# Performance work log

Measured on AMD Instinct MI355X. Metric: run time of the kernel, lower is better.

## Reference

```python
import jax, jax.numpy as jnp
import numpy as np

HIDDEN = 2048
NUM_HEADS = 16
HEAD_DIM = 128
WINDOW = 256
BATCH = 2
SEQ = 2048
ROPE_BASE = 10000.0


def apply_rope(t):
    # t: [b, h, s, d]; half-split (rotate-half) rotary embedding
    d = t.shape[-1]
    s = t.shape[-2]
    inv_freq = 1.0 / (ROPE_BASE ** (jnp.arange(0, d, 2, dtype=jnp.float32) / d))  # [d/2]
    freqs = jnp.arange(s, dtype=jnp.float32)[:, None] * inv_freq[None, :]          # [s, d/2]
    cos, sin = jnp.cos(freqs), jnp.sin(freqs)
    t1, t2 = t[..., : d // 2], t[..., d // 2 :]
    return jnp.concatenate([t1 * cos - t2 * sin, t1 * sin + t2 * cos], axis=-1)


def setup_inputs() -> dict:
    key = jax.random.key(0)
    ks = jax.random.split(key, 10)
    dm = HEAD_DIM * NUM_HEADS
    lin_std = 1.0 / np.sqrt(HIDDEN)
    out_std = 1.0 / np.sqrt(dm)
    return {
        "x": jax.random.normal(ks[0], (BATCH, SEQ, HIDDEN), dtype=jnp.float32),
        "W_Q": jax.random.uniform(ks[1], (HIDDEN, dm), jnp.float32, -lin_std, lin_std),
        "b_Q": jax.random.uniform(ks[2], (dm,), jnp.float32, -lin_std, lin_std),
        "W_K": jax.random.uniform(ks[3], (HIDDEN, dm), jnp.float32, -lin_std, lin_std),
        "b_K": jax.random.uniform(ks[4], (dm,), jnp.float32, -lin_std, lin_std),
        "W_V": jax.random.uniform(ks[5], (HIDDEN, dm), jnp.float32, -lin_std, lin_std),
        "b_V": jax.random.uniform(ks[6], (dm,), jnp.float32, -lin_std, lin_std),
        "W_O": jax.random.uniform(ks[7], (dm, HIDDEN), jnp.float32, -out_std, out_std),
        "b_O": jax.random.uniform(ks[8], (HIDDEN,), jnp.float32, -out_std, out_std),
        "key_weights": jax.random.normal(ks[9], (NUM_HEADS,), dtype=jnp.float32),
    }


def reference(x, W_Q, b_Q, W_K, b_K, W_V, b_V, W_O, b_O, key_weights):
    b, s, _ = x.shape
    scale = HEAD_DIM ** -0.5

    def split_heads(t):  # [b, s, h*d] -> [b, h, s, d]
        return t.reshape(b, s, NUM_HEADS, HEAD_DIM).transpose(0, 2, 1, 3)

    q = split_heads(x @ W_Q + b_Q)
    k = split_heads(x @ W_K + b_K)
    v = split_heads(x @ W_V + b_V)

    q = apply_rope(q)
    k = apply_rope(k)

    # num_kv_heads == num_heads here, so group_size == 1: plain per-head attention
    scores = jnp.einsum("bhqd,bhkd->bhqk", q, k) * scale
    scores = scores * key_weights[None, :, None, None]

    # sliding-window causal mask: allow 0 <= i - j <= WINDOW
    i = jnp.arange(s)[:, None]
    j = jnp.arange(s)[None, :]
    allowed = (j <= i) & (j >= i - WINDOW)
    scores = jnp.where(allowed[None, None], scores, -jnp.inf)

    attn = jax.nn.softmax(scores, axis=-1)
    out = jnp.einsum("bhqk,bhkd->bhqd", attn, v)  # [b, h, s, d]
    out = out.transpose(0, 2, 1, 3).reshape(b, s, NUM_HEADS * HEAD_DIM)
    return out @ W_O + b_O
```

## Files before the change

kernel.cpp:

```cpp
#include <hip/hip_runtime.h>
#include <cstdint>

#define SEQn   2048
#define NHn    16
#define HDn    128
#define DMn    2048
#define HIDn   2048
#define BATCHn 2
#define WINn   256
#define MROWS  (BATCHn*SEQn)
#define WELEMS ((size_t)HIDn * DMn)

typedef short s16x8 __attribute__((ext_vector_type(8)));
typedef float f32x4 __attribute__((ext_vector_type(4)));

__device__ __forceinline__ float bf2f(ushort x) {
    union { uint u; float f; } v; v.u = ((uint)x) << 16; return v.f;
}
__device__ __forceinline__ ushort f2bf(float f) {
    union { float f; uint u; } v; v.f = f;
    uint u = v.u;
    return (ushort)((u + 0x7FFFu + ((u >> 16) & 1u)) >> 16);
}

#define GLOAD_LDS16(g, l) __builtin_amdgcn_global_load_lds(                   \
    (const __attribute__((address_space(1))) unsigned int*)(g),               \
    (__attribute__((address_space(3))) unsigned int*)(l), 16, 0, 0)

#define FENCE() do { asm volatile("" ::: "memory");                           \
                     __builtin_amdgcn_sched_barrier(0); } while (0)

__global__ __launch_bounds__(256)
void transpose_all_kernel(const float* __restrict__ WQ, const float* __restrict__ WK,
                          const float* __restrict__ WV, const float* __restrict__ WO,
                          ushort* __restrict__ WT,
                          const float* __restrict__ x, ushort* __restrict__ xb)
{
    const int tid = threadIdx.y * 32 + threadIdx.x;
    if (blockIdx.z == 4) {
        const int bid = blockIdx.y * 64 + blockIdx.x;
        const size_t base = ((size_t)bid * 256 + tid) * 8;
        const float4 a0 = *reinterpret_cast<const float4*>(x + base);
        const float4 a1 = *reinterpret_cast<const float4*>(x + base + 4);
        ushort4 o0, o1;
        o0.x = f2bf(a0.x); o0.y = f2bf(a0.y); o0.z = f2bf(a0.z); o0.w = f2bf(a0.w);
        o1.x = f2bf(a1.x); o1.y = f2bf(a1.y); o1.z = f2bf(a1.z); o1.w = f2bf(a1.w);
        *reinterpret_cast<ushort4*>(xb + base)     = o0;
        *reinterpret_cast<ushort4*>(xb + base + 4) = o1;
        return;
    }
    __shared__ ushort t[32][33];
    const float* src = (blockIdx.z == 0) ? WQ : (blockIdx.z == 1) ? WK
                     : (blockIdx.z == 2) ? WV : WO;
    ushort* dst = WT + (size_t)blockIdx.z * WELEMS;
    const int tx = threadIdx.x, ty = threadIdx.y;
    const int n  = blockIdx.x * 32 + tx;
    const int k0 = blockIdx.y * 32;
    #pragma unroll
    for (int r = ty; r < 32; r += 8)
        t[r][tx] = f2bf(src[(size_t)(k0 + r) * 2048 + n]);
    __syncthreads();
    const int k  = k0 + tx;
    const int nb = blockIdx.x * 32;
    #pragma unroll
    for (int r = ty; r < 32; r += 8)
        dst[(size_t)(nb + r) * 2048 + k] = t[tx][r];
}

__global__ __launch_bounds__(256)
void transpose_cvt_kernel(const float* __restrict__ src, ushort* __restrict__ dst)
{
    __shared__ ushort t[32][33];
    const int tx = threadIdx.x, ty = threadIdx.y;
    const int n  = blockIdx.x * 32 + tx;
    const int k0 = blockIdx.y * 32;
    #pragma unroll
    for (int r = ty; r < 32; r += 8)
        t[r][tx] = f2bf(src[(size_t)(k0 + r) * 2048 + n]);
    __syncthreads();
    const int k  = k0 + tx;
    const int nb = blockIdx.x * 32;
    #pragma unroll
    for (int r = ty; r < 32; r += 8)
        dst[(size_t)(nb + r) * 2048 + k] = t[tx][r];
}

template<int ABF16>
__global__ __launch_bounds__(256)
void gemm_qkv_kernel(const void* __restrict__ Araw, const ushort* __restrict__ WT,
                     const float* __restrict__ bQ, const float* __restrict__ bK,
                     const float* __restrict__ bV,
                     ushort* __restrict__ Qb, ushort* __restrict__ Kb,
                     ushort* __restrict__ Vt)
{
    __shared__ __align__(16) ushort smem[32768];
    const int tid = threadIdx.x;
    const int m0  = blockIdx.y * 128;
    const int n0g = blockIdx.x * 128;
    const int sel = n0g >> 11;
    const int n0  = n0g & 2047;
    const ushort* BT  = WT + (size_t)sel * WELEMS;
    const float* bias = (sel == 0) ? bQ : (sel == 1) ? bK : bV;
    const int w  = tid >> 6;
    const int l  = tid & 63;
    const int wy = w >> 1, wx = w & 1;
    const int q  = l >> 4, lm = l & 15;
    const int sw = lm & 7;

    f32x4 acc[4][4];
    #pragma unroll
    for (int i = 0; i < 4; ++i)
        #pragma unroll
        for (int j = 0; j < 4; ++j) acc[i][j] = (f32x4)0.0f;

    auto stage = [&](int slot, int kt) {
        ushort* AsS = smem + slot * 16384;
        ushort* BsS = AsS + 8192;
        if (ABF16) {
            #pragma unroll
            for (int it = 0; it < 4; ++it) {
                const int v = it * 256 + tid;
                const int r = v >> 3;
                const int cs = ((v & 7) ^ (r & 7)) << 3;
                const ushort* gA = (const ushort*)Araw + (size_t)(m0 + r) * HIDn + kt + cs;
                const ushort* gB = BT + (size_t)(n0 + r) * HIDn + kt + cs;
                GLOAD_LDS16(gA, AsS + (it * 256 + w * 64) * 8);
                GLOAD_LDS16(gB, BsS + (it * 256 + w * 64) * 8);
            }
        } else {
            #pragma unroll
            for (int it = 0; it < 4; ++it) {
                const int v = it * 256 + tid;
                const int r = v >> 3;
                const int c = (v & 7) << 3;
                const float* Af = (const float*)Araw + (size_t)(m0 + r) * HIDn + kt + c;
                const float4 a0 = *reinterpret_cast<const float4*>(Af);
                const float4 a1 = *reinterpret_cast<const float4*>(Af + 4);
                ushort* d = &AsS[(size_t)(v ^ (r & 7)) * 8];
                d[0] = f2bf(a0.x); d[1] = f2bf(a0.y); d[2] = f2bf(a0.z); d[3] = f2bf(a0.w);
                d[4] = f2bf(a1.x); d[5] = f2bf(a1.y); d[6] = f2bf(a1.z); d[7] = f2bf(a1.w);
                const int cs = ((v & 7) ^ (r & 7)) << 3;
                const ushort* gB = BT + (size_t)(n0 + r) * HIDn + kt + cs;
                GLOAD_LDS16(gB, BsS + (it * 256 + w * 64) * 8);
            }
        }
    };

    auto compute = [&](int slot) {
        const ushort* AsS = smem + slot * 16384;
        const ushort* BsS = AsS + 8192;
        #pragma unroll
        for (int ks = 0; ks < 2; ++ks) {
            s16x8 af[4], bfv[4];
            #pragma unroll
            for (int im = 0; im < 4; ++im) {
                const int arow = wy * 64 + im * 16 + lm;
                af[im] = *reinterpret_cast<const s16x8*>(
                    &AsS[arow * 64 + (((ks * 4 + q) ^ sw) << 3)]);
            }
            #pragma unroll
            for (int in = 0; in < 4; ++in) {
                const int brow = wx * 64 + in * 16 + lm;
                bfv[in] = *reinterpret_cast<const s16x8*>(
                    &BsS[brow * 64 + (((ks * 4 + q) ^ sw) << 3)]);
            }
            __builtin_amdgcn_s_setprio(1);
            #pragma unroll
            for (int im = 0; im < 4; ++im)
                #pragma unroll
                for (int in = 0; in < 4; ++in)
                    acc[im][in] = __builtin_amdgcn_mfma_f32_16x16x32_bf16(af[im], bfv[in], acc[im][in], 0, 0, 0);
            __builtin_amdgcn_s_setprio(0);
        }
    };

    const int NT = HIDn / 64;
    stage(0, 0);
    int cur = 0;
    for (int t = 0; t < NT - 1; ++t) {
        stage(cur ^ 1, (t + 1) * 64);
        if (ABF16) asm volatile("s_waitcnt vmcnt(8)" ::: "memory");
        else       asm volatile("s_waitcnt vmcnt(4)" ::: "memory");
        __builtin_amdgcn_s_barrier();
        FENCE();
        compute(cur);
        FENCE();
        if (!ABF16) asm volatile("s_waitcnt lgkmcnt(0)" ::: "memory");
        __builtin_amdgcn_s_barrier();
        FENCE();
        cur ^= 1;
    }
    asm volatile("s_waitcnt vmcnt(0)" ::: "memory");
    __builtin_amdgcn_s_barrier();
    FENCE();
    compute(cur);
    __syncthreads();

    if (sel == 2) {
        ushort* ctile = smem;
        #pragma unroll
        for (int in = 0; in < 4; ++in) {
            const int col = wx * 64 + in * 16 + lm;
            const float bv = bias[n0 + col];
            #pragma unroll
            for (int im = 0; im < 4; ++im) {
                const int row0 = wy * 64 + im * 16 + q * 4;
                #pragma unroll
                for (int r = 0; r < 4; ++r)
                    ctile[col * 136 + row0 + r] = f2bf(acc[im][in][r] + bv);
            }
        }
        __syncthreads();
        const int hh = n0 >> 7;
        const int bb = m0 >> 11;
        const int s0 = m0 & (SEQn - 1);
        const int st = (tid & 15) * 8;
        const int d0 = tid >> 4;
        #pragma unroll
        for (int db = 0; db < 8; ++db) {
            const int d = d0 + db * 16;
            const ushort4 v0 = *reinterpret_cast<const ushort4*>(&ctile[d * 136 + st]);
            const ushort4 v1 = *reinterpret_cast<const ushort4*>(&ctile[d * 136 + st + 4]);
            ushort* dstp = Vt + (((size_t)(bb * NHn + hh)) * HDn + d) * SEQn + s0 + st;
            *reinterpret_cast<ushort4*>(dstp)     = v0;
            *reinterpret_cast<ushort4*>(dstp + 4) = v1;
        }
    } else {
        ushort* ctile = smem;
        #pragma unroll
        for (int in = 0; in < 4; ++in) {
            const int col = wx * 64 + in * 16 + lm;
            const float bv = bias[n0 + col];
            #pragma unroll
            for (int im = 0; im < 4; ++im) {
                const int row0 = wy * 64 + im * 16 + q * 4;
                #pragma unroll
                for (int r = 0; r < 4; ++r)
                    ctile[(row0 + r) * 136 + col] = f2bf(acc[im][in][r] + bv);
            }
        }
        __syncthreads();
        ushort* dst = (sel == 0) ? Qb : Kb;
        const int d = tid & 63;
        const float invf = exp2f(-(float)d * 0.20762050593046f);
        for (int r = tid >> 6; r < 128; r += 4) {
            const int s = (m0 + r) & (SEQn - 1);
            const float ang = (float)s * invf;
            float sn, cs;
            __sincosf(ang, &sn, &cs);
            const float t1 = bf2f(ctile[r * 136 + d]);
            const float t2 = bf2f(ctile[r * 136 + 64 + d]);
            const size_t base = (size_t)(m0 + r) * DMn + n0 + d;
            dst[base]      = f2bf(t1 * cs - t2 * sn);
            dst[base + 64] = f2bf(t1 * sn + t2 * cs);
        }
    }
}

__global__ __launch_bounds__(256)
void gemm_out_kernel(const ushort* __restrict__ A, const ushort* __restrict__ BT,
                     const float* __restrict__ bias, float* __restrict__ C)
{
    __shared__ __align__(16) ushort smem[24576];
    const int tid = threadIdx.x;
    const int m0 = blockIdx.y * 64;
    const int n0 = blockIdx.x * 128;
    const int w  = tid >> 6;
    const int l  = tid & 63;
    const int wy = w >> 1, wx = w & 1;
    const int q  = l >> 4, lm = l & 15;
    const int sw = lm & 7;

    f32x4 acc[2][4];
    #pragma unroll
    for (int i = 0; i < 2; ++i)
        #pragma unroll
        for (int j = 0; j < 4; ++j) acc[i][j] = (f32x4)0.0f;

    auto stage = [&](int slot, int kt) {
        ushort* AsS = smem + slot * 12288;
        ushort* BsS = AsS + 4096;
        #pragma unroll
        for (int it = 0; it < 2; ++it) {
            const int v = it * 256 + tid;
            const int r = v >> 3;
            const int cs = ((v & 7) ^ (r & 7)) << 3;
            GLOAD_LDS16(A + (size_t)(m0 + r) * DMn + kt + cs,
                        AsS + (it * 256 + w * 64) * 8);
        }
        #pragma unroll
        for (int it = 0; it < 4; ++it) {
            const int v = it * 256 + tid;
            const int r = v >> 3;
            const int cs = ((v & 7) ^ (r & 7)) << 3;
            GLOAD_LDS16(BT + (size_t)(n0 + r) * DMn + kt + cs,
                        BsS + (it * 256 + w * 64) * 8);
        }
    };

    auto compute = [&](int slot) {
        const ushort* AsS = smem + slot * 12288;
        const ushort* BsS = AsS + 4096;
        #pragma unroll
        for (int ks = 0; ks < 2; ++ks) {
            s16x8 af[2], bfv[4];
            #pragma unroll
            for (int im = 0; im < 2; ++im) {
                const int arow = wy * 32 + im * 16 + lm;
                af[im] = *reinterpret_cast<const s16x8*>(
                    &AsS[arow * 64 + (((ks * 4 + q) ^ sw) << 3)]);
            }
            #pragma unroll
            for (int in = 0; in < 4; ++in) {
                const int brow = wx * 64 + in * 16 + lm;
                bfv[in] = *reinterpret_cast<const s16x8*>(
                    &BsS[brow * 64 + (((ks * 4 + q) ^ sw) << 3)]);
            }
            __builtin_amdgcn_s_setprio(1);
            #pragma unroll
            for (int im = 0; im < 2; ++im)
                #pragma unroll
                for (int in = 0; in < 4; ++in)
                    acc[im][in] = __builtin_amdgcn_mfma_f32_16x16x32_bf16(af[im], bfv[in], acc[im][in], 0, 0, 0);
            __builtin_amdgcn_s_setprio(0);
        }
    };

    const int NT = DMn / 64;
    stage(0, 0);
    int cur = 0;
    for (int t = 0; t < NT - 1; ++t) {
        stage(cur ^ 1, (t + 1) * 64);
        asm volatile("s_waitcnt vmcnt(6)" ::: "memory");
        __builtin_amdgcn_s_barrier();
        FENCE();
        compute(cur);
        FENCE();
        __builtin_amdgcn_s_barrier();
        FENCE();
        cur ^= 1;
    }
    asm volatile("s_waitcnt vmcnt(0)" ::: "memory");
    __builtin_amdgcn_s_barrier();
    FENCE();
    compute(cur);

    #pragma unroll
    for (int in = 0; in < 4; ++in) {
        const int gcol = n0 + wx * 64 + in * 16 + lm;
        const float bv = bias[gcol];
        #pragma unroll
        for (int im = 0; im < 2; ++im) {
            const int grow0 = m0 + wy * 32 + im * 16 + q * 4;
            #pragma unroll
            for (int r = 0; r < 4; ++r)
                C[(size_t)(grow0 + r) * HIDn + gcol] = acc[im][in][r] + bv;
        }
    }
}

__global__ __launch_bounds__(256)
void attn_mfma_kernel(const ushort* Q, const ushort* __restrict__ K,
                      const ushort* __restrict__ Vt, const float* __restrict__ kw,
                      ushort* AO)
{
    __shared__ ushort plds[4][16 * 40];
    const int w  = threadIdx.x >> 6;
    const int l  = threadIdx.x & 63;
    const int q  = l >> 4, lm = l & 15;
    const int gw = blockIdx.x * 4 + w;
    const int qt = gw & 127;
    const int h  = (gw >> 7) & (NHn - 1);
    const int b  = gw >> 11;
    const int q0 = qt * 16;
    const float f = kw[h] * 0.08838834764831845f;

    s16x8 qf[4];
    const size_t qbase = ((size_t)(b * SEQn + q0 + lm)) * DMn + h * HDn;
    #pragma unroll
    for (int ks = 0; ks < 4; ++ks)
        qf[ks] = *reinterpret_cast<const s16x8*>(Q + qbase + ks * 32 + q * 8);

    f32x4 O[8];
    #pragma unroll
    for (int nt = 0; nt < 8; ++nt) O[nt] = (f32x4)0.0f;
    float m[4]    = {-1e30f, -1e30f, -1e30f, -1e30f};
    float lsum[4] = {0.f, 0.f, 0.f, 0.f};

    const int lo = q0 - WINn;
    const int c0 = lo > 0 ? (lo & ~31) : 0;
    const int nch = (q0 + 16 - c0 + 31) >> 5;

    const size_t kbh = ((size_t)(b * SEQn)) * DMn + h * HDn;
    const size_t vbh = ((size_t)(b * NHn + h)) * HDn * SEQn;

    for (int c = 0; c < nch; ++c) {
        const int kc = c0 + c * 32;
        s16x8 vf[8];
        #pragma unroll
        for (int nt = 0; nt < 8; ++nt)
            vf[nt] = *reinterpret_cast<const s16x8*>(
                Vt + vbh + (size_t)(nt * 16 + lm) * SEQn + kc + q * 8);
        f32x4 S[2];
        #pragma unroll
        for (int t = 0; t < 2; ++t) {
            f32x4 acc = (f32x4)0.0f;
            const size_t krow = kbh + (size_t)(kc + t * 16 + lm) * DMn;
            s16x8 kf[4];
            #pragma unroll
            for (int ks = 0; ks < 4; ++ks)
                kf[ks] = *reinterpret_cast<const s16x8*>(K + krow + ks * 32 + q * 8);
            __builtin_amdgcn_s_setprio(1);
            #pragma unroll
            for (int ks = 0; ks < 4; ++ks)
                acc = __builtin_amdgcn_mfma_f32_16x16x32_bf16(qf[ks], kf[ks], acc, 0, 0, 0);
            __builtin_amdgcn_s_setprio(0);
            S[t] = acc;
        }
        const int j0 = kc + lm, j1 = kc + 16 + lm;
        #pragma unroll
        for (int r = 0; r < 4; ++r) {
            const int i = q0 + q * 4 + r;
            float v0 = S[0][r] * f;
            float v1 = S[1][r] * f;
            if (j0 > i || j0 < i - WINn) v0 = -1e30f;
            if (j1 > i || j1 < i - WINn) v1 = -1e30f;
            float mx = fmaxf(v0, v1);
            #pragma unroll
            for (int off = 8; off > 0; off >>= 1)
                mx = fmaxf(mx, __shfl_xor(mx, off));
            const float mn = fmaxf(m[r], mx);
            const float alpha = __expf(m[r] - mn);
            m[r] = mn;
            const ushort h0 = f2bf(__expf(v0 - mn));
            const ushort h1 = f2bf(__expf(v1 - mn));
            plds[w][(q * 4 + r) * 40 + lm]      = h0;
            plds[w][(q * 4 + r) * 40 + 16 + lm] = h1;
            float ps = bf2f(h0) + bf2f(h1);
            #pragma unroll
            for (int off = 8; off > 0; off >>= 1)
                ps += __shfl_xor(ps, off);
            lsum[r] = lsum[r] * alpha + ps;
            #pragma unroll
            for (int nt = 0; nt < 8; ++nt) O[nt][r] *= alpha;
        }
        const s16x8 pf = *reinterpret_cast<const s16x8*>(&plds[w][lm * 40 + q * 8]);
        __builtin_amdgcn_s_setprio(1);
        #pragma unroll
        for (int nt = 0; nt < 8; ++nt)
            O[nt] = __builtin_amdgcn_mfma_f32_16x16x32_bf16(pf, vf[nt], O[nt], 0, 0, 0);
        __builtin_amdgcn_s_setprio(0);
    }
    #pragma unroll
    for (int r = 0; r < 4; ++r) {
        const float inv = 1.0f / lsum[r];
        const size_t orow = ((size_t)(b * SEQn + q0 + q * 4 + r)) * DMn + h * HDn;
        #pragma unroll
        for (int nt = 0; nt < 8; ++nt)
            AO[orow + nt * 16 + lm] = f2bf(O[nt][r] * inv);
    }
}

extern "C" void kernel_launch(void* const* d_in, const int* in_sizes, int n_in,
                              void* d_out, int out_size, void* d_ws, size_t ws_size,
                              hipStream_t stream)
{
    (void)in_sizes; (void)n_in; (void)out_size;
    const float* x  = (const float*)d_in[0];
    const float* WQ = (const float*)d_in[1];
    const float* bQ = (const float*)d_in[2];
    const float* WK = (const float*)d_in[3];
    const float* bK = (const float*)d_in[4];
    const float* WV = (const float*)d_in[5];
    const float* bV = (const float*)d_in[6];
    const float* WO = (const float*)d_in[7];
    const float* bO = (const float*)d_in[8];
    const float* kw = (const float*)d_in[9];
    float* out = (float*)d_out;

    char* ws = (char*)d_ws;
    const size_t AELEMS = (size_t)MROWS * DMn;
    ushort* Qb = (ushort*)ws;
    ushort* Kb = (ushort*)(ws + AELEMS * 2);
    ushort* Vt = (ushort*)(ws + AELEMS * 4);
    ushort* WT = (ushort*)(ws + AELEMS * 6);
    const size_t FULL = AELEMS * 6 + WELEMS * 8 + AELEMS * 2;
    const bool have_full = ws_size >= FULL;
    ushort* xb = (ushort*)(ws + AELEMS * 6 + WELEMS * 8);

    const dim3 tblk(32, 8);

    if (have_full) {
        transpose_all_kernel<<<dim3(64, 64, 5), tblk, 0, stream>>>(WQ, WK, WV, WO, WT, x, xb);
        gemm_qkv_kernel<1><<<dim3(3 * DMn / 128, MROWS / 128), 256, 0, stream>>>(
            xb, WT, bQ, bK, bV, Qb, Kb, Vt);
        attn_mfma_kernel<<<dim3(BATCHn * NHn * (SEQn / 16) / 4), 256, 0, stream>>>(Qb, Kb, Vt, kw, Qb);
        gemm_out_kernel<<<dim3(HIDn / 128, MROWS / 64), 256, 0, stream>>>(
            Qb, WT + 3 * WELEMS, bO, out);
    } else {
        transpose_all_kernel<<<dim3(64, 64, 3), tblk, 0, stream>>>(WQ, WK, WV, WO, WT, x, xb);
        gemm_qkv_kernel<0><<<dim3(3 * DMn / 128, MROWS / 128), 256, 0, stream>>>(
            x, WT, bQ, bK, bV, Qb, Kb, Vt);
        attn_mfma_kernel<<<dim3(BATCHn * NHn * (SEQn / 16) / 4), 256, 0, stream>>>(Qb, Kb, Vt, kw, Qb);
        transpose_cvt_kernel<<<dim3(64, 64), tblk, 0, stream>>>(WO, WT);
        gemm_out_kernel<<<dim3(HIDn / 128, MROWS / 64), 256, 0, stream>>>(Qb, WT, bO, out);
    }
}
```

Measured before the change: 374.5 us.

## Widen transpose tiles, enlarge out-GEMM tile, add block swizzles across kernels

```diff
diff --git a/kernel.cpp b/kernel.cpp
--- a/kernel.cpp
+++ b/kernel.cpp
@@ -38,33 +38,43 @@
 {
     const int tid = threadIdx.y * 32 + threadIdx.x;
     if (blockIdx.z == 4) {
-        const int bid = blockIdx.y * 64 + blockIdx.x;
-        const size_t base = ((size_t)bid * 256 + tid) * 8;
-        const float4 a0 = *reinterpret_cast<const float4*>(x + base);
-        const float4 a1 = *reinterpret_cast<const float4*>(x + base + 4);
-        ushort4 o0, o1;
-        o0.x = f2bf(a0.x); o0.y = f2bf(a0.y); o0.z = f2bf(a0.z); o0.w = f2bf(a0.w);
-        o1.x = f2bf(a1.x); o1.y = f2bf(a1.y); o1.z = f2bf(a1.z); o1.w = f2bf(a1.w);
-        *reinterpret_cast<ushort4*>(xb + base)     = o0;
-        *reinterpret_cast<ushort4*>(xb + base + 4) = o1;
+        const int bid = blockIdx.y * 32 + blockIdx.x;
+        const size_t b0 = (size_t)bid * 8192;
+        #pragma unroll
+        for (int i = 0; i < 4; ++i) {
+            const size_t base = b0 + i * 2048 + tid * 8;
+            const float4 a0 = *reinterpret_cast<const float4*>(x + base);
+            const float4 a1 = *reinterpret_cast<const float4*>(x + base + 4);
+            ushort4 o0, o1;
+            o0.x = f2bf(a0.x); o0.y = f2bf(a0.y); o0.z = f2bf(a0.z); o0.w = f2bf(a0.w);
+            o1.x = f2bf(a1.x); o1.y = f2bf(a1.y); o1.z = f2bf(a1.z); o1.w = f2bf(a1.w);
+            *reinterpret_cast<ushort4*>(xb + base)     = o0;
+            *reinterpret_cast<ushort4*>(xb + base + 4) = o1;
+        }
         return;
     }
-    __shared__ ushort t[32][33];
+    __shared__ ushort t[64][72];
     const float* src = (blockIdx.z == 0) ? WQ : (blockIdx.z == 1) ? WK
                      : (blockIdx.z == 2) ? WV : WO;
     ushort* dst = WT + (size_t)blockIdx.z * WELEMS;
-    const int tx = threadIdx.x, ty = threadIdx.y;
-    const int n  = blockIdx.x * 32 + tx;
-    const int k0 = blockIdx.y * 32;
-    #pragma unroll
-    for (int r = ty; r < 32; r += 8)
-        t[r][tx] = f2bf(src[(size_t)(k0 + r) * 2048 + n]);
+    const int n0 = blockIdx.x * 64;
+    const int k0 = blockIdx.y * 64;
+    const int c  = tid & 63;
+    const int rr = tid >> 6;
+    #pragma unroll
+    for (int i = 0; i < 16; ++i) {
+        const int r = i * 4 + rr;
+        t[c][r] = f2bf(src[(size_t)(k0 + r) * 2048 + n0 + c]);
+    }
     __syncthreads();
-    const int k  = k0 + tx;
-    const int nb = blockIdx.x * 32;
-    #pragma unroll
-    for (int r = ty; r < 32; r += 8)
-        dst[(size_t)(nb + r) * 2048 + k] = t[tx][r];
+    const int rowg = tid >> 4;
+    const int kc   = (tid & 15) * 4;
+    #pragma unroll
+    for (int rr2 = 0; rr2 < 4; ++rr2) {
+        const int arow = rowg + rr2 * 16;
+        const ushort4 v = *reinterpret_cast<const ushort4*>(&t[arow][kc]);
+        *reinterpret_cast<ushort4*>(dst + (size_t)(n0 + arow) * 2048 + k0 + kc) = v;
+    }
 }
 
 __global__ __launch_bounds__(256)
@@ -95,8 +105,10 @@
 {
     __shared__ __align__(16) ushort smem[32768];
     const int tid = threadIdx.x;
-    const int m0  = blockIdx.y * 128;
-    const int n0g = blockIdx.x * 128;
+    const int lin = blockIdx.y * 48 + blockIdx.x;
+    const int swz = (lin & 7) * 192 + (lin >> 3);
+    const int m0  = (swz / 48) * 128;
+    const int n0g = (swz % 48) * 128;
     const int sel = n0g >> 11;
     const int n0  = n0g & 2047;
     const ushort* BT  = WT + (size_t)sel * WELEMS;
@@ -261,52 +273,48 @@
 void gemm_out_kernel(const ushort* __restrict__ A, const ushort* __restrict__ BT,
                      const float* __restrict__ bias, float* __restrict__ C)
 {
-    __shared__ __align__(16) ushort smem[24576];
+    __shared__ __align__(16) ushort smem[32768];
     const int tid = threadIdx.x;
-    const int m0 = blockIdx.y * 64;
-    const int n0 = blockIdx.x * 128;
+    const int lin = blockIdx.y * 16 + blockIdx.x;
+    const int swz = (lin & 7) * 64 + (lin >> 3);
+    const int m0 = (swz >> 4) * 128;
+    const int n0 = (swz & 15) * 128;
     const int w  = tid >> 6;
     const int l  = tid & 63;
     const int wy = w >> 1, wx = w & 1;
     const int q  = l >> 4, lm = l & 15;
     const int sw = lm & 7;
 
-    f32x4 acc[2][4];
-    #pragma unroll
-    for (int i = 0; i < 2; ++i)
+    f32x4 acc[4][4];
+    #pragma unroll
+    for (int i = 0; i < 4; ++i)
         #pragma unroll
         for (int j = 0; j < 4; ++j) acc[i][j] = (f32x4)0.0f;
 
     auto stage = [&](int slot, int kt) {
-        ushort* AsS = smem + slot * 12288;
-        ushort* BsS = AsS + 4096;
-        #pragma unroll
-        for (int it = 0; it < 2; ++it) {
-            const int v = it * 256 + tid;
-            const int r = v >> 3;
-            const int cs = ((v & 7) ^ (r & 7)) << 3;
-            GLOAD_LDS16(A + (size_t)(m0 + r) * DMn + kt + cs,
-                        AsS + (it * 256 + w * 64) * 8);
-        }
+        ushort* AsS = smem + slot * 16384;
+        ushort* BsS = AsS + 8192;
         #pragma unroll
         for (int it = 0; it < 4; ++it) {
             const int v = it * 256 + tid;
             const int r = v >> 3;
             const int cs = ((v & 7) ^ (r & 7)) << 3;
+            GLOAD_LDS16(A  + (size_t)(m0 + r) * DMn + kt + cs,
+                        AsS + (it * 256 + w * 64) * 8);
             GLOAD_LDS16(BT + (size_t)(n0 + r) * DMn + kt + cs,
                         BsS + (it * 256 + w * 64) * 8);
         }
     };
 
     auto compute = [&](int slot) {
-        const ushort* AsS = smem + slot * 12288;
-        const ushort* BsS = AsS + 4096;
+        const ushort* AsS = smem + slot * 16384;
+        const ushort* BsS = AsS + 8192;
         #pragma unroll
         for (int ks = 0; ks < 2; ++ks) {
-            s16x8 af[2], bfv[4];
-            #pragma unroll
-            for (int im = 0; im < 2; ++im) {
-                const int arow = wy * 32 + im * 16 + lm;
+            s16x8 af[4], bfv[4];
+            #pragma unroll
+            for (int im = 0; im < 4; ++im) {
+                const int arow = wy * 64 + im * 16 + lm;
                 af[im] = *reinterpret_cast<const s16x8*>(
                     &AsS[arow * 64 + (((ks * 4 + q) ^ sw) << 3)]);
             }
@@ -318,7 +326,7 @@
             }
             __builtin_amdgcn_s_setprio(1);
             #pragma unroll
-            for (int im = 0; im < 2; ++im)
+            for (int im = 0; im < 4; ++im)
                 #pragma unroll
                 for (int in = 0; in < 4; ++in)
                     acc[im][in] = __builtin_amdgcn_mfma_f32_16x16x32_bf16(af[im], bfv[in], acc[im][in], 0, 0, 0);
@@ -331,7 +339,7 @@
     int cur = 0;
     for (int t = 0; t < NT - 1; ++t) {
         stage(cur ^ 1, (t + 1) * 64);
-        asm volatile("s_waitcnt vmcnt(6)" ::: "memory");
+        asm volatile("s_waitcnt vmcnt(8)" ::: "memory");
         __builtin_amdgcn_s_barrier();
         FENCE();
         compute(cur);
@@ -350,8 +358,8 @@
         const int gcol = n0 + wx * 64 + in * 16 + lm;
         const float bv = bias[gcol];
         #pragma unroll
-        for (int im = 0; im < 2; ++im) {
-            const int grow0 = m0 + wy * 32 + im * 16 + q * 4;
+        for (int im = 0; im < 4; ++im) {
+            const int grow0 = m0 + wy * 64 + im * 16 + q * 4;
             #pragma unroll
             for (int r = 0; r < 4; ++r)
                 C[(size_t)(grow0 + r) * HIDn + gcol] = acc[im][in][r] + bv;
@@ -368,7 +376,9 @@
     const int w  = threadIdx.x >> 6;
     const int l  = threadIdx.x & 63;
     const int q  = l >> 4, lm = l & 15;
-    const int gw = blockIdx.x * 4 + w;
+    const int bid = blockIdx.x;
+    const int swzb = (bid & 7) * 128 + (bid >> 3);
+    const int gw = swzb * 4 + w;
     const int qt = gw & 127;
     const int h  = (gw >> 7) & (NHn - 1);
     const int b  = gw >> 11;
@@ -491,18 +501,18 @@
     const dim3 tblk(32, 8);
 
     if (have_full) {
-        transpose_all_kernel<<<dim3(64, 64, 5), tblk, 0, stream>>>(WQ, WK, WV, WO, WT, x, xb);
+        transpose_all_kernel<<<dim3(32, 32, 5), tblk, 0, stream>>>(WQ, WK, WV, WO, WT, x, xb);
         gemm_qkv_kernel<1><<<dim3(3 * DMn / 128, MROWS / 128), 256, 0, stream>>>(
             xb, WT, bQ, bK, bV, Qb, Kb, Vt);
         attn_mfma_kernel<<<dim3(BATCHn * NHn * (SEQn / 16) / 4), 256, 0, stream>>>(Qb, Kb, Vt, kw, Qb);
-        gemm_out_kernel<<<dim3(HIDn / 128, MROWS / 64), 256, 0, stream>>>(
+        gemm_out_kernel<<<dim3(HIDn / 128, MROWS / 128), 256, 0, stream>>>(
             Qb, WT + 3 * WELEMS, bO, out);
     } else {
-        transpose_all_kernel<<<dim3(64, 64, 3), tblk, 0, stream>>>(WQ, WK, WV, WO, WT, x, xb);
+        transpose_all_kernel<<<dim3(32, 32, 3), tblk, 0, stream>>>(WQ, WK, WV, WO, WT, x, xb);
         gemm_qkv_kernel<0><<<dim3(3 * DMn / 128, MROWS / 128), 256, 0, stream>>>(
             x, WT, bQ, bK, bV, Qb, Kb, Vt);
         attn_mfma_kernel<<<dim3(BATCHn * NHn * (SEQn / 16) / 4), 256, 0, stream>>>(Qb, Kb, Vt, kw, Qb);
         transpose_cvt_kernel<<<dim3(64, 64), tblk, 0, stream>>>(WO, WT);
-        gemm_out_kernel<<<dim3(HIDn / 128, MROWS / 64), 256, 0, stream>>>(Qb, WT, bO, out);
-    }
-}
+        gemm_out_kernel<<<dim3(HIDn / 128, MROWS / 128), 256, 0, stream>>>(Qb, WT, bO, out);
+    }
+}
```

New measurement: 381.3 us. Within noise of the previous version (+1.8%).
